# Performance work log

Measured on AMD Instinct MI355X. Metric: run time of the kernel, lower is better.

The kernel has to match this reference:

```python
import jax, jax.numpy as jnp
import numpy as np

T = 2048
D_MODEL = 4096
N_HEADS = 32
N_GROUPS = 8
HEAD_DIM = 128


def _rope_tables(tokens, head_dim, base=10000.0):
    inv_freq = 1.0 / (base ** (np.arange(0, head_dim, 2, dtype=np.float32) / head_dim))
    pos = np.arange(tokens, dtype=np.float32)
    freqs = np.einsum('t,d->td', pos, inv_freq)          # [T, D/2]
    emb = np.concatenate([freqs, freqs], axis=-1)         # [T, D]
    return jnp.asarray(np.cos(emb)), jnp.asarray(np.sin(emb))


def setup_inputs() -> dict:
    key = jax.random.key(0)
    k1, k2, k3 = jax.random.split(key, 3)
    x = jax.random.normal(k1, (T, D_MODEL), dtype=jnp.float32)
    w_qkv = jax.random.normal(k2, (D_MODEL, (N_HEADS + 2 * N_GROUPS) * HEAD_DIM), dtype=jnp.float32) * 0.02
    w_out = jax.random.normal(k3, (N_HEADS * HEAD_DIM, D_MODEL), dtype=jnp.float32) * 0.02
    cos, sin = _rope_tables(T, HEAD_DIM)
    mask = jnp.tril(jnp.ones((T, T), dtype=bool))  # causal: [suffix_tokens, total_tokens]
    return {"x": x, "w_qkv": w_qkv, "w_out": w_out, "cos": cos, "sin": sin, "mask": mask}


def _rotate_half(u):
    u1, u2 = jnp.split(u, 2, axis=-1)
    return jnp.concatenate([-u2, u1], axis=-1)


def _apply_rope(u, cos, sin):
    # u: [tokens, heads, head_dim]; cos/sin: [tokens, head_dim]
    c = cos[:, None, :]
    s = sin[:, None, :]
    return u * c + _rotate_half(u) * s


def reference(x, w_qkv, w_out, cos, sin, mask):
    group_dim = N_HEADS // N_GROUPS
    qkv = x @ w_qkv                                        # [T, (H+2G)*D]
    q, k, v = jnp.split(qkv, [N_HEADS * HEAD_DIM, (N_HEADS + N_GROUPS) * HEAD_DIM], axis=-1)
    q = q.reshape(T, N_HEADS, HEAD_DIM)
    k = k.reshape(T, N_GROUPS, HEAD_DIM)
    v = v.reshape(T, N_GROUPS, HEAD_DIM)
    q = _apply_rope(q, cos, sin)
    k = _apply_rope(k, cos, sin)
    # GQA: group queries -> [T, G, group_dim, D]
    qg = q.reshape(T, N_GROUPS, group_dim, HEAD_DIM)
    scale = 1.0 / jnp.sqrt(jnp.asarray(HEAD_DIM, dtype=q.dtype))
    scores = jnp.einsum('tghd,sgd->ghts', qg, k) * scale   # [G, gd, T, S]
    neg = jnp.asarray(jnp.finfo(scores.dtype).min, scores.dtype)
    scores = jnp.where(mask[None, None, :, :], scores, neg)
    probs = jax.nn.softmax(scores, axis=-1)
    out = jnp.einsum('ghts,sgd->tghd', probs, v)           # [T, G, gd, D]
    out = out.reshape(T, N_HEADS * HEAD_DIM)
    return out @ w_out                                     # [T, model_dim]
```

## Files before the change

### kernel.cpp

```cpp
#include <hip/hip_runtime.h>
#include <cstdint>
#include <cstddef>

#define TT   2048
#define DM   4096
#define NH   32
#define NG   8
#define HD   128
#define QKVN 6144
#define KOFF 4096
#define VOFF 5120

typedef __attribute__((ext_vector_type(8))) short bf16x8;
typedef __attribute__((ext_vector_type(4))) float f32x4;
typedef unsigned short u16;

__device__ __forceinline__ u16 f2b(float f) {
  unsigned u = __builtin_bit_cast(unsigned, f);
  u += 0x7fffu + ((u >> 16) & 1u);
  return (u16)(u >> 16);
}
__device__ __forceinline__ float b2f(u16 s) {
  unsigned u = ((unsigned)s) << 16;
  return __builtin_bit_cast(float, u);
}

__device__ __forceinline__ void gload_lds16(const void* g, void* l) {
  __builtin_amdgcn_global_load_lds(
      (const __attribute__((address_space(1))) unsigned int*)g,
      (__attribute__((address_space(3))) unsigned int*)l,
      16, 0, 0);
}

__global__ __launch_bounds__(256) void cvt_f32_bf16(
    const float* __restrict__ src, u16* __restrict__ dst, int n) {
  for (int i = (blockIdx.x * 256 + threadIdx.x) * 4; i < n; i += gridDim.x * 256 * 4) {
    float4 v = *(const float4*)(src + i);
    ushort4 o;
    o.x = f2b(v.x); o.y = f2b(v.y); o.z = f2b(v.z); o.w = f2b(v.w);
    *(ushort4*)(dst + i) = o;
  }
}

__global__ __launch_bounds__(256) void transpose_cvt(
    const float* __restrict__ src, u16* __restrict__ dst, int R, int C) {
  __shared__ __align__(16) u16 tile[64 * 68];
  const int rb = blockIdx.y * 64, cb = blockIdx.x * 64;
  const int tid = threadIdx.x;
#pragma unroll
  for (int it = 0; it < 4; ++it) {
    const int idx = it * 256 + tid;
    const int r = idx >> 4, c4 = (idx & 15) * 4;
    const float4 v = *(const float4*)(src + (size_t)(rb + r) * C + cb + c4);
    tile[(c4 + 0) * 68 + r] = f2b(v.x);
    tile[(c4 + 1) * 68 + r] = f2b(v.y);
    tile[(c4 + 2) * 68 + r] = f2b(v.z);
    tile[(c4 + 3) * 68 + r] = f2b(v.w);
  }
  __syncthreads();
#pragma unroll
  for (int it = 0; it < 4; ++it) {
    const int idx = it * 256 + tid;
    const int c = idx >> 4, r4 = (idx & 15) * 4;
    const ushort4 o = *(const ushort4*)&tile[c * 68 + r4];
    *(ushort4*)(dst + (size_t)(cb + c) * R + rb + r4) = o;
  }
}

template <int WN, bool OUT_BF16>
__global__ __launch_bounds__(512) void gemm8p(
    const u16* __restrict__ A, const u16* __restrict__ Bt, void* __restrict__ Cout,
    int M, int N, int K) {
  __shared__ __align__(16) u16 sA[2][128 * 64];
  __shared__ __align__(16) u16 sB[2][WN * 64 * 64];
  const int tid = threadIdx.x;
  const int wid = tid >> 6, lane = tid & 63;
  const int lane15 = lane & 15, laneh = lane >> 4;
  const int wm = wid >> 2, wn = wid & 3;
  const int bid = blockIdx.x;
  const int xcd = bid & 7, j = bid >> 3;
  const int m0 = ((xcd >> 1) * 4 + (j >> 3)) * 128;
  const int n0 = ((xcd & 1) * 8 + (j & 7)) * (WN * 64);
  const int xorL = (lane15 & 7) << 3;

  f32x4 acc[4][WN];
#pragma unroll
  for (int m = 0; m < 4; ++m)
#pragma unroll
    for (int n = 0; n < WN; ++n)
#pragma unroll
      for (int r = 0; r < 4; ++r) acc[m][n][r] = 0.f;

  auto stageA = [&](int buf, int t) {
    const int k0 = t << 6;
#pragma unroll
    for (int i = 0; i < 2; ++i) {
      const int ebase = (wid * 2 + i) * 512;
      const int e = ebase + lane * 8;
      const int row = e >> 6;
      const int col = (e & 63) ^ ((row & 7) << 3);
      gload_lds16(A + (size_t)(m0 + row) * K + k0 + col, &sA[buf][ebase]);
    }
  };
  auto stageB = [&](int buf, int t) {
    const int k0 = t << 6;
#pragma unroll
    for (int i = 0; i < WN; ++i) {
      const int ebase = (wid * WN + i) * 512;
      const int e = ebase + lane * 8;
      const int row = e >> 6;
      const int col = (e & 63) ^ ((row & 7) << 3);
      gload_lds16(Bt + (size_t)(n0 + row) * K + k0 + col, &sB[buf][ebase]);
    }
  };

  const int NT = K >> 6;
  stageA(0, 0);
  stageB(0, 0);
  stageA(1, 1);
  asm volatile("s_waitcnt vmcnt(2)");
  __builtin_amdgcn_s_barrier();

  for (int u = 0; u < NT; ++u) {
    const int cur = u & 1;
    bf16x8 af[4][2], bfr[WN][2];
#pragma unroll
    for (int m = 0; m < 4; ++m)
#pragma unroll
      for (int ks = 0; ks < 2; ++ks)
        af[m][ks] = *(const bf16x8*)&sA[cur][(wm * 64 + m * 16 + lane15) * 64 +
                                            ((ks * 32 + laneh * 8) ^ xorL)];
#pragma unroll
    for (int n = 0; n < WN / 2; ++n)
#pragma unroll
      for (int ks = 0; ks < 2; ++ks)
        bfr[n][ks] = *(const bf16x8*)&sB[cur][(wn * (WN * 16) + n * 16 + lane15) * 64 +
                                             ((ks * 32 + laneh * 8) ^ xorL)];
    if (u + 1 < NT) stageB(cur ^ 1, u + 1);
    __builtin_amdgcn_sched_barrier(0);
    __builtin_amdgcn_s_setprio(1);
#pragma unroll
    for (int ks = 0; ks < 2; ++ks)
#pragma unroll
      for (int m = 0; m < 4; ++m)
#pragma unroll
        for (int n = 0; n < WN / 2; ++n)
          acc[m][n] = __builtin_amdgcn_mfma_f32_16x16x32_bf16(af[m][ks], bfr[n][ks], acc[m][n], 0, 0, 0);
    __builtin_amdgcn_s_setprio(0);
    __builtin_amdgcn_s_barrier();
#pragma unroll
    for (int n = WN / 2; n < WN; ++n)
#pragma unroll
      for (int ks = 0; ks < 2; ++ks)
        bfr[n][ks] = *(const bf16x8*)&sB[cur][(wn * (WN * 16) + n * 16 + lane15) * 64 +
                                             ((ks * 32 + laneh * 8) ^ xorL)];
    if (u + 2 < NT) stageA(cur, u + 2);
    __builtin_amdgcn_sched_barrier(0);
    __builtin_amdgcn_s_setprio(1);
#pragma unroll
    for (int ks = 0; ks < 2; ++ks)
#pragma unroll
      for (int m = 0; m < 4; ++m)
#pragma unroll
        for (int n = WN / 2; n < WN; ++n)
          acc[m][n] = __builtin_amdgcn_mfma_f32_16x16x32_bf16(af[m][ks], bfr[n][ks], acc[m][n], 0, 0, 0);
    __builtin_amdgcn_s_setprio(0);
    if (u + 2 < NT) asm volatile("s_waitcnt vmcnt(2)");
    else            asm volatile("s_waitcnt vmcnt(0)");
    __builtin_amdgcn_s_barrier();
  }
#pragma unroll
  for (int m = 0; m < 4; ++m)
#pragma unroll
    for (int n = 0; n < WN; ++n)
#pragma unroll
      for (int r = 0; r < 4; ++r) {
        const int row = m0 + wm * 64 + m * 16 + laneh * 4 + r;
        const int col = n0 + wn * (WN * 16) + n * 16 + lane15;
        const float v = acc[m][n][r];
        if (OUT_BF16) ((u16*)Cout)[(size_t)row * N + col] = f2b(v);
        else          ((float*)Cout)[(size_t)row * N + col] = v;
      }
}

__global__ __launch_bounds__(256) void rope_rearrange(
    const u16* __restrict__ qkv, const float* __restrict__ cosT,
    const float* __restrict__ sinT, u16* __restrict__ Qr, u16* __restrict__ Kr) {
  const int u = blockIdx.x * 4 + (threadIdx.x >> 6);
  const int lane = threadIdx.x & 63;
  const int t = u & (TT - 1);
  const int e = u >> 11;
  const u16* in;
  u16* outp;
  if (e < NH) {
    in = qkv + (size_t)t * QKVN + e * HD;
    outp = Qr + ((size_t)e * TT + t) * HD;
  } else {
    const int g = e - NH;
    in = qkv + (size_t)t * QKVN + KOFF + g * HD;
    outp = Kr + ((size_t)g * TT + t) * HD;
  }
  const float u1 = b2f(in[lane]), u2 = b2f(in[lane + 64]);
  const float c1 = cosT[t * HD + lane], s1 = sinT[t * HD + lane];
  const float c2 = cosT[t * HD + lane + 64], s2 = sinT[t * HD + lane + 64];
  outp[lane]      = f2b(u1 * c1 - u2 * s1);
  outp[lane + 64] = f2b(u2 * c2 + u1 * s2);
}

__global__ __launch_bounds__(256) void vtrans(
    const u16* __restrict__ qkv, u16* __restrict__ VT) {
  __shared__ u16 tile[64][66];
  const int g = blockIdx.z;
  const int t0 = blockIdx.x * 64, d0 = blockIdx.y * 64;
  const int tid = threadIdx.x;
#pragma unroll
  for (int it = 0; it < 16; ++it) {
    int idx = it * 256 + tid;
    int i = idx >> 6, j = idx & 63;
    tile[i][j] = qkv[(size_t)(t0 + i) * QKVN + VOFF + g * HD + d0 + j];
  }
  __syncthreads();
#pragma unroll
  for (int it = 0; it < 16; ++it) {
    int idx = it * 256 + tid;
    int j = idx >> 6, i = idx & 63;
    VT[((size_t)g * HD + d0 + j) * TT + t0 + i] = tile[i][j];
  }
}

__global__ __launch_bounds__(512) void attn(
    const u16* __restrict__ Qr, const u16* __restrict__ Kr,
    const u16* __restrict__ VT, u16* __restrict__ AO) {
  __shared__ __align__(16) u16 sK[2][128 * 128];
  __shared__ __align__(16) u16 sV[2][128 * 128];
  __shared__ __align__(16) u16 sP[8][16 * 128];
  const int bid = blockIdx.x;
  const int swz = (bid & 7) * 32 + (bid >> 3);
  const int h = swz >> 3, p = swz & 7;
  const int g = h >> 2;
  const int tid = threadIdx.x, wid = tid >> 6, lane = tid & 63;
  const int lane15 = lane & 15, laneh = lane >> 4;
  const int xorL = (lane15 & 7) << 3;
  const u16* Qh = Qr + (size_t)h * TT * HD;
  const u16* Kg = Kr + (size_t)g * TT * HD;
  const u16* Vg = VT + (size_t)g * HD * TT;
  const float scale = 0.08838834764831845f;

  auto stageKV = [&](int buf, int kv) {
#pragma unroll
    for (int i = 0; i < 4; ++i) {
      const int ebase = (wid * 4 + i) * 512;
      const int e = ebase + lane * 8;
      const int row = e >> 7;
      const int col = (e & 127) ^ ((row & 7) << 3);
      gload_lds16(Kg + (size_t)(kv * 128 + row) * HD + col, &sK[buf][ebase]);
      gload_lds16(Vg + (size_t)row * TT + kv * 128 + col, &sV[buf][ebase]);
    }
  };

  for (int pass = 0; pass < 2; ++pass) {
    const int qt = pass ? (15 - p) : p;
    bf16x8 qf[4];
    const int qrow0 = qt * 128 + wid * 16;
#pragma unroll
    for (int ks = 0; ks < 4; ++ks)
      qf[ks] = *(const bf16x8*)(Qh + (size_t)(qrow0 + lane15) * HD + ks * 32 + laneh * 8);

    f32x4 acc_o[8];
    float mrow[4], lrow[4];
#pragma unroll
    for (int n = 0; n < 8; ++n)
#pragma unroll
      for (int r = 0; r < 4; ++r) acc_o[n][r] = 0.f;
#pragma unroll
    for (int r = 0; r < 4; ++r) { mrow[r] = -1e30f; lrow[r] = 0.f; }

    stageKV(0, 0);
    for (int kv = 0; kv <= qt; ++kv) {
      const int cur = kv & 1;
      if (kv < qt) stageKV(cur ^ 1, kv + 1);
      __builtin_amdgcn_sched_barrier(0);
      if (kv < qt) asm volatile("s_waitcnt vmcnt(8)");
      else         asm volatile("s_waitcnt vmcnt(0)");
      __builtin_amdgcn_s_barrier();

      f32x4 s[8];
#pragma unroll
      for (int n = 0; n < 8; ++n)
#pragma unroll
        for (int r = 0; r < 4; ++r) s[n][r] = 0.f;
      __builtin_amdgcn_s_setprio(1);
#pragma unroll
      for (int ks = 0; ks < 4; ++ks) {
        bf16x8 kf[8];
#pragma unroll
        for (int n = 0; n < 8; ++n)
          kf[n] = *(const bf16x8*)&sK[cur][(n * 16 + lane15) * 128 + ((ks * 32 + laneh * 8) ^ xorL)];
#pragma unroll
        for (int n = 0; n < 8; ++n)
          s[n] = __builtin_amdgcn_mfma_f32_16x16x32_bf16(qf[ks], kf[n], s[n], 0, 0, 0);
      }
      __builtin_amdgcn_s_setprio(0);

      if (kv == qt) {
#pragma unroll
        for (int n = 0; n < 8; ++n)
#pragma unroll
          for (int r = 0; r < 4; ++r) {
            const int ql = wid * 16 + laneh * 4 + r;
            const int sl = n * 16 + lane15;
            s[n][r] = (sl > ql) ? -1e30f : s[n][r] * scale;
          }
      } else {
#pragma unroll
        for (int n = 0; n < 8; ++n)
#pragma unroll
          for (int r = 0; r < 4; ++r) s[n][r] *= scale;
      }
#pragma unroll
      for (int r = 0; r < 4; ++r) {
        float pm = s[0][r];
#pragma unroll
        for (int n = 1; n < 8; ++n) pm = fmaxf(pm, s[n][r]);
        pm = fmaxf(pm, __shfl_xor(pm, 1));
        pm = fmaxf(pm, __shfl_xor(pm, 2));
        pm = fmaxf(pm, __shfl_xor(pm, 4));
        pm = fmaxf(pm, __shfl_xor(pm, 8));
        const float mnew = fmaxf(mrow[r], pm);
        const float corr = __expf(mrow[r] - mnew);
        mrow[r] = mnew;
        float ps = 0.f;
#pragma unroll
        for (int n = 0; n < 8; ++n) {
          const float pr = __expf(s[n][r] - mnew);
          s[n][r] = pr;
          ps += pr;
        }
        ps += __shfl_xor(ps, 1); ps += __shfl_xor(ps, 2);
        ps += __shfl_xor(ps, 4); ps += __shfl_xor(ps, 8);
        lrow[r] = lrow[r] * corr + ps;
#pragma unroll
        for (int n = 0; n < 8; ++n) acc_o[n][r] *= corr;
      }
#pragma unroll
      for (int n = 0; n < 8; ++n)
#pragma unroll
        for (int r = 0; r < 4; ++r) {
          const int prow = laneh * 4 + r;
          const int pcol = (n * 16 + lane15) ^ ((prow & 7) << 3);
          sP[wid][prow * 128 + pcol] = f2b(s[n][r]);
        }
      __builtin_amdgcn_s_setprio(1);
#pragma unroll
      for (int ks = 0; ks < 4; ++ks) {
        bf16x8 pf, vf[8];
        pf = *(const bf16x8*)&sP[wid][lane15 * 128 + ((ks * 32 + laneh * 8) ^ xorL)];
#pragma unroll
        for (int n = 0; n < 8; ++n)
          vf[n] = *(const bf16x8*)&sV[cur][(n * 16 + lane15) * 128 + ((ks * 32 + laneh * 8) ^ xorL)];
#pragma unroll
        for (int n = 0; n < 8; ++n)
          acc_o[n] = __builtin_amdgcn_mfma_f32_16x16x32_bf16(pf, vf[n], acc_o[n], 0, 0, 0);
      }
      __builtin_amdgcn_s_setprio(0);
      __builtin_amdgcn_s_barrier();
    }
    float inv[4];
#pragma unroll
    for (int r = 0; r < 4; ++r) inv[r] = 1.f / lrow[r];
#pragma unroll
    for (int n = 0; n < 8; ++n)
#pragma unroll
      for (int r = 0; r < 4; ++r) {
        const int trow = qt * 128 + wid * 16 + laneh * 4 + r;
        AO[(size_t)trow * DM + h * HD + n * 16 + lane15] = f2b(acc_o[n][r] * inv[r]);
      }
  }
}

extern "C" void kernel_launch(void* const* d_in, const int* in_sizes, int n_in,
                              void* d_out, int out_size, void* d_ws, size_t ws_size,
                              hipStream_t stream) {
  const float* x     = (const float*)d_in[0];
  const float* w_qkv = (const float*)d_in[1];
  const float* w_out = (const float*)d_in[2];
  const float* cosT  = (const float*)d_in[3];
  const float* sinT  = (const float*)d_in[4];
  float* out = (float*)d_out;

  char* ws = (char*)d_ws;
  u16* wT  = (u16*)(ws);
  u16* xb  = (u16*)(ws + 50331648);
  u16* qkv = (u16*)(ws + 50331648 + 16777216);
  u16* Qr  = (u16*)(ws + 50331648 + 16777216 + 25165824);
  u16* Kr  = Qr + (size_t)NH * TT * HD;
  u16* VT  = Kr + (size_t)NG * TT * HD;
  u16* AO  = xb;

  cvt_f32_bf16<<<2048, 256, 0, stream>>>(x, xb, TT * DM);
  transpose_cvt<<<dim3(QKVN / 64, DM / 64), 256, 0, stream>>>(w_qkv, wT, DM, QKVN);
  gemm8p<6, true><<<dim3((TT / 128) * (QKVN / 384)), 512, 0, stream>>>(
      xb, wT, qkv, TT, QKVN, DM);
  rope_rearrange<<<(TT * (NH + NG)) / 4, 256, 0, stream>>>(qkv, cosT, sinT, Qr, Kr);
  vtrans<<<dim3(TT / 64, HD / 64, NG), 256, 0, stream>>>(qkv, VT);
  transpose_cvt<<<dim3(DM / 64, DM / 64), 256, 0, stream>>>(w_out, wT, DM, DM);
  attn<<<NH * 8, 512, 0, stream>>>(Qr, Kr, VT, AO);
  gemm8p<4, false><<<dim3((TT / 128) * (DM / 256)), 512, 0, stream>>>(
      AO, wT, out, TT, DM, DM);
}
```

Before: 321.5 us.

## Triple-buffer A tiles and collapse GEMM main loop to one barrier

The A operand shared-memory staging goes from two buffers to three with a rotating index. This lets the next B tile and the A tile two steps ahead be issued at the top of each iteration. The split half-B load/compute phases with a mid-iteration barrier are merged into one fragment load, one MFMA block and one barrier per K step. This is meant to cut synchronization stalls and issue global prefetches earlier, at the cost of more LDS use and more live B fragment registers.

Result: slower. 347.8 us (+8.2%).

```diff
diff --git a/kernel.cpp b/kernel.cpp
--- a/kernel.cpp
+++ b/kernel.cpp
@@ -71,7 +71,7 @@
 __global__ __launch_bounds__(512) void gemm8p(
     const u16* __restrict__ A, const u16* __restrict__ Bt, void* __restrict__ Cout,
     int M, int N, int K) {
-  __shared__ __align__(16) u16 sA[2][128 * 64];
+  __shared__ __align__(16) u16 sA[3][128 * 64];
   __shared__ __align__(16) u16 sB[2][WN * 64 * 64];
   const int tid = threadIdx.x;
   const int wid = tid >> 6, lane = tid & 63;
@@ -121,22 +121,24 @@
   asm volatile("s_waitcnt vmcnt(2)");
   __builtin_amdgcn_s_barrier();
 
+  int curA = 0;
   for (int u = 0; u < NT; ++u) {
-    const int cur = u & 1;
+    const int curB = u & 1;
+    if (u + 1 < NT) stageB(curB ^ 1, u + 1);
+    if (u + 2 < NT) stageA(curA == 0 ? 2 : curA - 1, u + 2);
     bf16x8 af[4][2], bfr[WN][2];
 #pragma unroll
     for (int m = 0; m < 4; ++m)
 #pragma unroll
       for (int ks = 0; ks < 2; ++ks)
-        af[m][ks] = *(const bf16x8*)&sA[cur][(wm * 64 + m * 16 + lane15) * 64 +
-                                            ((ks * 32 + laneh * 8) ^ xorL)];
-#pragma unroll
-    for (int n = 0; n < WN / 2; ++n)
+        af[m][ks] = *(const bf16x8*)&sA[curA][(wm * 64 + m * 16 + lane15) * 64 +
+                                             ((ks * 32 + laneh * 8) ^ xorL)];
+#pragma unroll
+    for (int n = 0; n < WN; ++n)
 #pragma unroll
       for (int ks = 0; ks < 2; ++ks)
-        bfr[n][ks] = *(const bf16x8*)&sB[cur][(wn * (WN * 16) + n * 16 + lane15) * 64 +
-                                             ((ks * 32 + laneh * 8) ^ xorL)];
-    if (u + 1 < NT) stageB(cur ^ 1, u + 1);
+        bfr[n][ks] = *(const bf16x8*)&sB[curB][(wn * (WN * 16) + n * 16 + lane15) * 64 +
+                                              ((ks * 32 + laneh * 8) ^ xorL)];
     __builtin_amdgcn_sched_barrier(0);
     __builtin_amdgcn_s_setprio(1);
 #pragma unroll
@@ -144,30 +146,13 @@
 #pragma unroll
       for (int m = 0; m < 4; ++m)
 #pragma unroll
-        for (int n = 0; n < WN / 2; ++n)
-          acc[m][n] = __builtin_amdgcn_mfma_f32_16x16x32_bf16(af[m][ks], bfr[n][ks], acc[m][n], 0, 0, 0);
-    __builtin_amdgcn_s_setprio(0);
-    __builtin_amdgcn_s_barrier();
-#pragma unroll
-    for (int n = WN / 2; n < WN; ++n)
-#pragma unroll
-      for (int ks = 0; ks < 2; ++ks)
-        bfr[n][ks] = *(const bf16x8*)&sB[cur][(wn * (WN * 16) + n * 16 + lane15) * 64 +
-                                             ((ks * 32 + laneh * 8) ^ xorL)];
-    if (u + 2 < NT) stageA(cur, u + 2);
-    __builtin_amdgcn_sched_barrier(0);
-    __builtin_amdgcn_s_setprio(1);
-#pragma unroll
-    for (int ks = 0; ks < 2; ++ks)
-#pragma unroll
-      for (int m = 0; m < 4; ++m)
-#pragma unroll
-        for (int n = WN / 2; n < WN; ++n)
+        for (int n = 0; n < WN; ++n)
           acc[m][n] = __builtin_amdgcn_mfma_f32_16x16x32_bf16(af[m][ks], bfr[n][ks], acc[m][n], 0, 0, 0);
     __builtin_amdgcn_s_setprio(0);
     if (u + 2 < NT) asm volatile("s_waitcnt vmcnt(2)");
     else            asm volatile("s_waitcnt vmcnt(0)");
     __builtin_amdgcn_s_barrier();
+    curA = (curA == 2) ? 0 : curA + 1;
   }
 #pragma unroll
   for (int m = 0; m < 4; ++m)
```
